# Kernel tuning notes

Measured on AMD Instinct MI355X. Metric: run time of the kernel, lower is better.

The kernel has to match this reference:

```python
import jax, jax.numpy as jnp
import numpy as np

# dims: O=1 templates/chains, L=384 residues, d_pair=d_bias=128, 4 heads x 32
O, L, DP, DB, H, DH = 1, 384, 128, 128, 4, 32
SCALING = 1.0 / np.sqrt(DH)


def _ln(x, g, b):
    # torch nn.LayerNorm over last dim, eps=1e-5, biased variance
    m = jnp.mean(x, axis=-1, keepdims=True)
    v = jnp.mean((x - m) ** 2, axis=-1, keepdims=True)
    return (x - m) * jax.lax.rsqrt(v + 1e-5) * g + b


def setup_inputs() -> dict:
    key = jax.random.key(0)
    ks = jax.random.split(key, 9)

    def w(k, shape, s=0.02):
        return (jax.random.normal(k, shape) * s).astype(jnp.float32)

    return {
        "pair": jax.random.normal(ks[0], (O, L, L, DP), dtype=jnp.float32),
        "bias": jax.random.normal(ks[1], (O, L, L, DB), dtype=jnp.float32),
        "ln_pair_g": jnp.ones((DP,), jnp.float32),
        "ln_pair_b": jnp.zeros((DP,), jnp.float32),
        "ln_bias_g": jnp.ones((DB,), jnp.float32),
        "ln_bias_b": jnp.zeros((DB,), jnp.float32),
        "Wq": w(ks[2], (H * DH, DP)),  # torch Linear weight layout (out, in)
        "Wk": w(ks[3], (H * DH, DP)),
        "Wv": w(ks[4], (H * DH, DP)),
        "Wb": w(ks[5], (H, DB)),
        "Wg": w(ks[6], (H * DH, DP)),
        "bg": jnp.ones((H * DH,), jnp.float32),
        "Wo": w(ks[7], (DP, H * DH)),
        "bo": w(ks[8], (DP,)),
    }


def reference(pair, bias, ln_pair_g, ln_pair_b, ln_bias_g, ln_bias_b,
              Wq, Wk, Wv, Wb, Wg, bg, Wo, bo):
    # is_row=True: swap the two L axes so attention runs along rows
    p = jnp.transpose(pair, (0, 2, 1, 3))   # [O, L, L, DP]
    bsrc = jnp.transpose(bias, (0, 2, 1, 3))  # [O, L, L, DB]

    p = _ln(p, ln_pair_g, ln_pair_b)
    bsrc = _ln(bsrc, ln_bias_g, ln_bias_b)

    q = (p @ Wq.T).reshape(O, L, L, H, DH) * SCALING
    k = (p @ Wk.T).reshape(O, L, L, H, DH) / L
    v = (p @ Wv.T).reshape(O, L, L, H, DH)
    b = bsrc @ Wb.T                         # [O, L, L, H] pairwise bias
    gate = jax.nn.sigmoid(p @ Wg.T + bg)    # [O, L, L, H*DH]

    # attention scores contracted over the non-attended axial dim n and head dim k
    attn = jnp.einsum('bnihk,bnjhk->bijh', q, k) + b
    attn = jax.nn.softmax(attn, axis=2)     # softmax over j (torch dim=-2)

    out = jnp.einsum('bijh,bnjhd->bnihd', attn, v).reshape(O, L, L, H * DH)
    out = (gate * out) @ Wo.T + bo          # [O, L, L, DP]
    return jnp.transpose(out, (0, 2, 1, 3))  # undo is_row permute
```

## Files before the change

kernel.cpp:

```cpp
#include <hip/hip_runtime.h>
#include <hip/hip_bf16.h>

#define L_DIM 384
#define DPC 128
#define NH 4
#define DHD 32
#define HD 128
#define NROWS (L_DIM*L_DIM)
#define NSPLIT 16

#define SB_BF16 32768
#define SB_Q 0
#define SB_K 8192
#define SB_G 16384
#define SB_V 24576

typedef __hip_bfloat16 bf16;
typedef __attribute__((ext_vector_type(8))) short bf8_t;
typedef __attribute__((ext_vector_type(4))) short bf4_t;
typedef __attribute__((ext_vector_type(4))) float f4_t;

__device__ __forceinline__ float bf2f(bf16 x){ return __bfloat162float(x); }
__device__ __forceinline__ bf16 f2bf(float x){ return __float2bfloat16(x); }

union bfu8 { bf8_t v; bf16 h[8]; };

__global__ __launch_bounds__(256) void k_prep(
    const float* __restrict__ Wq, const float* __restrict__ Wk, const float* __restrict__ Wv,
    const float* __restrict__ Wg, const float* __restrict__ Wo,
    bf16* __restrict__ Wqp, bf16* __restrict__ Wkp, bf16* __restrict__ Wvp,
    bf16* __restrict__ Wgp, bf16* __restrict__ Wop)
{
  const int o = blockIdx.x * 256 + threadIdx.x;
  const int j = o & 7, lane = (o >> 3) & 63, ks = (o >> 9) & 3, nt = o >> 11;
  const int src = (nt*16 + (lane & 15))*DPC + ks*32 + (lane >> 4)*8 + j;
  Wqp[o] = f2bf(Wq[src]);
  Wkp[o] = f2bf(Wk[src]);
  Wvp[o] = f2bf(Wv[src]);
  Wgp[o] = f2bf(Wg[src]);
  Wop[o] = f2bf(Wo[src]);
}

__global__ __launch_bounds__(256) void k_bias_proj(
    const float* __restrict__ bias, const float* __restrict__ lng, const float* __restrict__ lnb,
    const float* __restrict__ Wb, float* __restrict__ bscore)
{
  const int tid = threadIdx.x;
  const int wave = tid >> 6, lane = tid & 63;
  const int sub = lane >> 4, l16 = lane & 15, c = l16 * 8;
  const int t = blockIdx.x * 16 + wave * 4 + sub;
  const int j = t / L_DIM, i = t % L_DIM;

  const float4 ga = *(const float4*)&lng[c], gb = *(const float4*)&lng[c+4];
  const float4 ba = *(const float4*)&lnb[c], bb = *(const float4*)&lnb[c+4];
  const float4 xa = *(const float4*)&bias[(size_t)t * DPC + c];
  const float4 xb = *(const float4*)&bias[(size_t)t * DPC + c + 4];

  float s  = xa.x+xa.y+xa.z+xa.w + xb.x+xb.y+xb.z+xb.w;
  float ss = xa.x*xa.x+xa.y*xa.y+xa.z*xa.z+xa.w*xa.w
           + xb.x*xb.x+xb.y*xb.y+xb.z*xb.z+xb.w*xb.w;
  #pragma unroll
  for (int off = 8; off; off >>= 1) { s += __shfl_xor(s, off, 64); ss += __shfl_xor(ss, off, 64); }
  const float mean = s * (1.f/128.f);
  const float var  = ss * (1.f/128.f) - mean*mean;
  const float rstd = rsqrtf(var + 1e-5f);
  float y[8];
  y[0]=(xa.x-mean)*rstd*ga.x+ba.x; y[1]=(xa.y-mean)*rstd*ga.y+ba.y;
  y[2]=(xa.z-mean)*rstd*ga.z+ba.z; y[3]=(xa.w-mean)*rstd*ga.w+ba.w;
  y[4]=(xb.x-mean)*rstd*gb.x+bb.x; y[5]=(xb.y-mean)*rstd*gb.y+bb.y;
  y[6]=(xb.z-mean)*rstd*gb.z+bb.z; y[7]=(xb.w-mean)*rstd*gb.w+bb.w;

  float p[4];
  #pragma unroll
  for (int h = 0; h < 4; ++h) {
    const float4 wa = *(const float4*)&Wb[h*DPC + c];
    const float4 wb4 = *(const float4*)&Wb[h*DPC + c + 4];
    p[h] = y[0]*wa.x + y[1]*wa.y + y[2]*wa.z + y[3]*wa.w
         + y[4]*wb4.x + y[5]*wb4.y + y[6]*wb4.z + y[7]*wb4.w;
    #pragma unroll
    for (int off = 8; off; off >>= 1) p[h] += __shfl_xor(p[h], off, 64);
  }
  if (l16 == 0) {
    #pragma unroll
    for (int h = 0; h < 4; ++h)
      bscore[((size_t)h*L_DIM + i)*L_DIM + j] = p[h];
  }
}

__global__ __launch_bounds__(256, 6) void k_pair_proj(
    const float* __restrict__ pair, const float* __restrict__ lng, const float* __restrict__ lnb,
    const bf16* __restrict__ Wqp, const bf16* __restrict__ Wkp, const bf16* __restrict__ Wvp,
    const bf16* __restrict__ Wgp, const float* __restrict__ bg,
    bf16* __restrict__ fused)
{
  __shared__ __align__(16) bf16 Sh[4 * 3072];
  const int tid = threadIdx.x;
  const int wave = tid >> 6, lane = tid & 63;
  bf16* WS = Sh + wave * 3072;
  const int i6 = blockIdx.x / 384, n = blockIdx.x % 384;
  const int i0g = i6*64 + wave*16;
  const int m = lane & 15, q4 = lane >> 4;

  bf16* SB = fused + ((size_t)n*6 + i6) * SB_BF16;

  {
    const int half = lane >> 5, l32 = lane & 31, c = l32 * 4;
    const float4 g4 = *(const float4*)&lng[c];
    const float4 b4 = *(const float4*)&lnb[c];
    float4 xv[8];
    #pragma unroll
    for (int rr = 0; rr < 8; ++rr)
      xv[rr] = *(const float4*)&pair[((size_t)(i0g + rr*2 + half)*L_DIM + n)*DPC + c];
    #pragma unroll
    for (int rr = 0; rr < 8; ++rr) {
      const int r = rr*2 + half;
      float s  = xv[rr].x + xv[rr].y + xv[rr].z + xv[rr].w;
      float ss = xv[rr].x*xv[rr].x + xv[rr].y*xv[rr].y + xv[rr].z*xv[rr].z + xv[rr].w*xv[rr].w;
      #pragma unroll
      for (int off = 16; off; off >>= 1) { s += __shfl_xor(s, off, 64); ss += __shfl_xor(ss, off, 64); }
      const float mean = s * (1.f/128.f);
      const float var  = ss * (1.f/128.f) - mean*mean;
      const float rstd = rsqrtf(var + 1e-5f);
      union { bf16 h[4]; bf4_t v; } pk;
      pk.h[0] = f2bf((xv[rr].x-mean)*rstd*g4.x + b4.x);
      pk.h[1] = f2bf((xv[rr].y-mean)*rstd*g4.y + b4.y);
      pk.h[2] = f2bf((xv[rr].z-mean)*rstd*g4.z + b4.z);
      pk.h[3] = f2bf((xv[rr].w-mean)*rstd*g4.w + b4.w);
      *(bf4_t*)&WS[r*136 + c] = pk.v;
    }
  }

  bf8_t afr[4];
  #pragma unroll
  for (int ks = 0; ks < 4; ++ks)
    afr[ks] = *(const bf8_t*)&WS[m*136 + ks*32 + q4*8];

  const bf16* W3[3] = {Wqp, Wkp, Wgp};
  const int soff3[3] = {SB_Q, SB_K, SB_G};
  #pragma unroll
  for (int s3 = 0; s3 < 3; ++s3) {
    const bf16* Wp = W3[s3];
    #pragma unroll
    for (int h = 0; h < 4; ++h) {
      f4_t acc0 = {0.f,0.f,0.f,0.f}, acc1 = {0.f,0.f,0.f,0.f};
      #pragma unroll
      for (int ks = 0; ks < 4; ++ks) {
        bf8_t b0 = *(const bf8_t*)&Wp[((h*2    )*4 + ks)*512 + lane*8];
        bf8_t b1 = *(const bf8_t*)&Wp[((h*2 + 1)*4 + ks)*512 + lane*8];
        acc0 = __builtin_amdgcn_mfma_f32_16x16x32_bf16(afr[ks], b0, acc0, 0, 0, 0);
        acc1 = __builtin_amdgcn_mfma_f32_16x16x32_bf16(afr[ks], b1, acc1, 0, 0, 0);
      }
      if (s3 == 2) {
        const float bg0 = bg[h*32 + m], bg1 = bg[h*32 + 16 + m];
        #pragma unroll
        for (int reg = 0; reg < 4; ++reg) {
          acc0[reg] = 1.f / (1.f + __expf(-(acc0[reg] + bg0)));
          acc1[reg] = 1.f / (1.f + __expf(-(acc1[reg] + bg1)));
        }
      }
      #pragma unroll
      for (int reg = 0; reg < 4; ++reg) {
        WS[(q4*4 + reg)*40 + m]      = f2bf(acc0[reg]);
        WS[(q4*4 + reg)*40 + 16 + m] = f2bf(acc1[reg]);
      }
      bf8_t fv = *(const bf8_t*)&WS[m*40 + q4*8];
      *(bf8_t*)&SB[soff3[s3] + (h*4 + wave)*512 + lane*8] = fv;
    }
  }

  #pragma unroll
  for (int nt = 0; nt < 8; ++nt) {
    f4_t acc = {0.f,0.f,0.f,0.f};
    #pragma unroll
    for (int ks = 0; ks < 4; ++ks) {
      bf8_t bfr = *(const bf8_t*)&Wvp[(nt*4 + ks)*512 + lane*8];
      acc = __builtin_amdgcn_mfma_f32_16x16x32_bf16(afr[ks], bfr, acc, 0, 0, 0);
    }
    #pragma unroll
    for (int reg = 0; reg < 4; ++reg)
      WS[(nt*16 + m)*24 + q4*4 + reg] = f2bf(acc[reg]);
  }
  const int Jloc = wave >> 1;
  const int wo = (wave & 1) * 32;
  #pragma unroll
  for (int st = 0; st < 4; ++st) {
    const int fid = st*2 + (lane >> 5);
    const int h = fid >> 1, dt = fid & 1;
    const int lnl = lane & 31;
    bf8_t val = *(const bf8_t*)&WS[(h*32 + dt*16 + (lnl & 15))*24 + (lnl >> 4)*8];
    *(bf8_t*)&SB[SB_V + (((Jloc*4 + h)*2 + dt)*512) + (wo + lnl)*8] = val;
  }
}

__global__ __launch_bounds__(256) void k_qk(
    const bf16* __restrict__ fused, float* __restrict__ Spart)
{
  const int tid = threadIdx.x, wave = tid >> 6, lane = tid & 63;
  const int m = lane & 15, q4 = lane >> 4;
  const int b = blockIdx.x;
  const int ks = b / 36, rem = b % 36;
  const int h = rem / 9, t9 = rem % 9;
  const int i0 = (t9/3)*128, j0 = (t9%3)*128;
  const int wr = (wave >> 1)*64, wc = (wave & 1)*64;

  f4_t acc[4][4];
  #pragma unroll
  for (int a = 0; a < 4; ++a)
    #pragma unroll
    for (int c = 0; c < 4; ++c) acc[a][c] = (f4_t){0.f,0.f,0.f,0.f};

  const bf16* qp = fused + ((size_t)(ks*24)*6 + ((i0 + wr) >> 6))*SB_BF16
                         + SB_Q + h*2048 + (size_t)lane*8;
  const bf16* kp = fused + ((size_t)(ks*24)*6 + ((j0 + wc) >> 6))*SB_BF16
                         + SB_K + h*2048 + (size_t)lane*8;
  const size_t nstride = (size_t)6*SB_BF16;

  bf8_t af[4], bfr[4];
  #pragma unroll
  for (int x = 0; x < 4; ++x) {
    af[x]  = *(const bf8_t*)(qp + x*512);
    bfr[x] = *(const bf8_t*)(kp + x*512);
  }
  #pragma unroll 2
  for (int kt = 0; kt < 24; ++kt) {
    bf8_t afn[4], bfn[4];
    if (kt < 23) {
      const bf16* qn = qp + (size_t)(kt+1)*nstride;
      const bf16* kn = kp + (size_t)(kt+1)*nstride;
      #pragma unroll
      for (int x = 0; x < 4; ++x) {
        afn[x] = *(const bf8_t*)(qn + x*512);
        bfn[x] = *(const bf8_t*)(kn + x*512);
      }
    }
    #pragma unroll
    for (int mt = 0; mt < 4; ++mt)
      #pragma unroll
      for (int nt = 0; nt < 4; ++nt)
        acc[mt][nt] = __builtin_amdgcn_mfma_f32_16x16x32_bf16(af[mt], bfr[nt], acc[mt][nt], 0, 0, 0);
    #pragma unroll
    for (int x = 0; x < 4; ++x) { af[x] = afn[x]; bfr[x] = bfn[x]; }
  }
  float* Sp = Spart + ((size_t)(ks*NH + h)*9 + t9)*16384;
  #pragma unroll
  for (int mt = 0; mt < 4; ++mt)
    #pragma unroll
    for (int nt = 0; nt < 4; ++nt)
      #pragma unroll
      for (int reg = 0; reg < 4; ++reg) {
        int il = wr + mt*16 + q4*4 + reg;
        int jl = wc + nt*16 + m;
        Sp[il*128 + jl] = acc[mt][nt][reg];
      }
}

__global__ __launch_bounds__(192) void k_softmax(
    const float* __restrict__ Spart, const float* __restrict__ bscore, bf16* __restrict__ attnf)
{
  const int t = threadIdx.x, wave = t >> 6, lane = t & 63;
  const int h = blockIdx.x / L_DIM, i = blockIdx.x % L_DIM;
  const float sc = 0.17677669529663687f / 384.f;
  const size_t toff = ((size_t)((i >> 7)*3 + wave))*16384 + (size_t)(i & 127)*128 + (t & 63)*2;

  float ax = 0.f, ay = 0.f;
  #pragma unroll
  for (int ksp = 0; ksp < NSPLIT; ++ksp) {
    float2 p = *(const float2*)&Spart[((size_t)(ksp*NH + h)*9)*16384 + toff];
    ax += p.x; ay += p.y;
  }
  const size_t off = ((size_t)h*L_DIM + i)*L_DIM + t*2;
  const float2 bs = *(const float2*)&bscore[off];
  ax = ax*sc + bs.x;
  ay = ay*sc + bs.y;

  __shared__ float redm[3], reds[3];
  float mx = fmaxf(ax, ay);
  #pragma unroll
  for (int o = 32; o; o >>= 1) mx = fmaxf(mx, __shfl_xor(mx, o, 64));
  if (lane == 0) redm[wave] = mx;
  __syncthreads();
  mx = fmaxf(fmaxf(redm[0], redm[1]), redm[2]);
  float ex = __expf(ax - mx), ey = __expf(ay - mx);
  float sm = ex + ey;
  #pragma unroll
  for (int o = 32; o; o >>= 1) sm += __shfl_xor(sm, o, 64);
  if (lane == 0) reds[wave] = sm;
  __syncthreads();
  const float inv = 1.f / (reds[0] + reds[1] + reds[2]);

  const int j = t*2;
  const int I = i >> 4, mm = i & 15, J = j >> 5, q4 = (j >> 3) & 3, jj = j & 7;
  union { bf16 h2[2]; unsigned u; } pk;
  pk.h2[0] = f2bf(ex * inv);
  pk.h2[1] = f2bf(ey * inv);
  size_t a = ((((size_t)h*24 + I)*12 + J)*64 + q4*16 + mm)*8 + jj;
  *(unsigned*)&attnf[a] = pk.u;
}

__global__ __launch_bounds__(256) void k_pv(
    const bf16* __restrict__ attnf, const bf16* __restrict__ fused,
    bf16* __restrict__ goutf)
{
  __shared__ __align__(16) bf16 Cs2[384*40];
  const int tid = threadIdx.x, wave = tid >> 6, lane = tid & 63;
  const int m = lane & 15, q4 = lane >> 4;
  const int n = blockIdx.x >> 2, h = blockIdx.x & 3;

  bf8_t ugp[6];
  #pragma unroll
  for (int it = 0; it < 6; ++it) {
    int u = tid + it*256;
    int I = u >> 6, ln = u & 63;
    ugp[it] = *(const bf8_t*)&fused[((size_t)n*6 + (I>>2))*SB_BF16 + SB_G
                                    + (h*4 + (I&3))*512 + ln*8];
  }

  f4_t acc[6][2];
  #pragma unroll
  for (int a = 0; a < 6; ++a) { acc[a][0] = (f4_t){0,0,0,0}; acc[a][1] = (f4_t){0,0,0,0}; }

  for (int J = 0; J < 12; ++J) {
    const bf16* vb = fused + ((size_t)n*6 + (J>>1))*SB_BF16 + SB_V
                           + (((J&1)*4 + h)*2)*512;
    bf8_t b0 = *(const bf8_t*)&vb[lane*8];
    bf8_t b1 = *(const bf8_t*)&vb[512 + lane*8];
    #pragma unroll
    for (int mt = 0; mt < 6; ++mt) {
      const int I = wave*6 + mt;
      bf8_t af = *(const bf8_t*)&attnf[(((size_t)h*24 + I)*12 + J)*512 + (size_t)lane*8];
      acc[mt][0] = __builtin_amdgcn_mfma_f32_16x16x32_bf16(af, b0, acc[mt][0], 0, 0, 0);
      acc[mt][1] = __builtin_amdgcn_mfma_f32_16x16x32_bf16(af, b1, acc[mt][1], 0, 0, 0);
    }
  }
  #pragma unroll
  for (int mt = 0; mt < 6; ++mt)
    #pragma unroll
    for (int dt = 0; dt < 2; ++dt)
      #pragma unroll
      for (int reg = 0; reg < 4; ++reg) {
        int i_loc = 16*(wave*6 + mt) + q4*4 + reg;
        Cs2[i_loc*40 + dt*16 + m] = f2bf(acc[mt][dt][reg]);
      }
  __syncthreads();
  #pragma unroll
  for (int it = 0; it < 6; ++it) {
    int u = tid + it*256;
    int I = u >> 6, ln = u & 63;
    bfu8 uc, ug, uo;
    uc.v = *(const bf8_t*)&Cs2[(I*16 + (ln&15))*40 + (ln>>4)*8];
    ug.v = ugp[it];
    #pragma unroll
    for (int e = 0; e < 8; ++e) uo.h[e] = f2bf(bf2f(uc.h[e]) * bf2f(ug.h[e]));
    size_t gidx = ((((size_t)n*24 + I)*NH + h)*64 + ln)*8;
    *(bf8_t*)&goutf[gidx] = uo.v;
  }
}

__global__ __launch_bounds__(256) void k_out(
    const bf16* __restrict__ goutf, const bf16* __restrict__ Wop, const float* __restrict__ bo,
    float* __restrict__ outp)
{
  __shared__ __align__(16) float Cs[64][132];
  const int tid = threadIdx.x, wave = tid >> 6, lane = tid & 63;
  const int m = lane & 15, q4 = lane >> 4;
  const int i0 = (blockIdx.x / 384) * 64, n = blockIdx.x % 384;

  bf8_t afr[4];
  #pragma unroll
  for (int ks = 0; ks < 4; ++ks)
    afr[ks] = *(const bf8_t*)&goutf[((((size_t)n*24 + (i0>>4) + wave)*NH + ks)*64 + lane)*8];

  #pragma unroll
  for (int nt = 0; nt < 8; ++nt) {
    f4_t acc = {0.f, 0.f, 0.f, 0.f};
    #pragma unroll
    for (int ks = 0; ks < 4; ++ks) {
      bf8_t bfr = *(const bf8_t*)&Wop[(nt*4 + ks)*512 + lane*8];
      acc = __builtin_amdgcn_mfma_f32_16x16x32_bf16(afr[ks], bfr, acc, 0, 0, 0);
    }
    const int col = nt*16 + m;
    const float bov = bo[col];
    #pragma unroll
    for (int reg = 0; reg < 4; ++reg)
      Cs[wave*16 + q4*4 + reg][col] = acc[reg] + bov;
  }
  __syncthreads();
  for (int u = tid; u < 2048; u += 256) {
    int r = u >> 5, c4 = (u & 31) * 4;
    size_t off = ((size_t)(i0 + r)*L_DIM + n)*DPC + c4;
    *(float4*)&outp[off] = *(const float4*)&Cs[r][c4];
  }
}

extern "C" void kernel_launch(void* const* d_in, const int* in_sizes, int n_in,
                              void* d_out, int out_size, void* d_ws, size_t ws_size,
                              hipStream_t stream)
{
  (void)in_sizes; (void)n_in; (void)out_size; (void)ws_size;
  const float* pair = (const float*)d_in[0];
  const float* bias = (const float*)d_in[1];
  const float* lnpg = (const float*)d_in[2];
  const float* lnpb = (const float*)d_in[3];
  const float* lnbg = (const float*)d_in[4];
  const float* lnbb = (const float*)d_in[5];
  const float* Wq   = (const float*)d_in[6];
  const float* Wk   = (const float*)d_in[7];
  const float* Wv   = (const float*)d_in[8];
  const float* Wb   = (const float*)d_in[9];
  const float* Wg   = (const float*)d_in[10];
  const float* bg   = (const float*)d_in[11];
  const float* Wo   = (const float*)d_in[12];
  const float* bo   = (const float*)d_in[13];
  float* outp = (float*)d_out;

  char* ws = (char*)d_ws;
  const size_t FUSED_SZ = (size_t)2304 * SB_BF16 * 2;
  bf16* fusedb  = (bf16*)(ws);
  float* bscore = (float*)(ws + FUSED_SZ);
  float* Spart  = (float*)(ws + FUSED_SZ + (size_t)NH*L_DIM*L_DIM*4);
  bf16*  attnf  = (bf16*)(ws + FUSED_SZ + (size_t)NH*L_DIM*L_DIM*4
                             + (size_t)NSPLIT*NH*L_DIM*L_DIM*4);
  char*  wb     = ws + FUSED_SZ + (size_t)NH*L_DIM*L_DIM*4
                     + (size_t)NSPLIT*NH*L_DIM*L_DIM*4 + (size_t)NH*L_DIM*L_DIM*2;
  bf16* Wqp = (bf16*)(wb);
  bf16* Wkp = (bf16*)(wb + 32768);
  bf16* Wvp = (bf16*)(wb + 65536);
  bf16* Wgp = (bf16*)(wb + 98304);
  bf16* Wop = (bf16*)(wb + 131072);
  bf16* goutf = (bf16*)Spart;

  hipLaunchKernelGGL(k_prep, dim3(64), dim3(256), 0, stream, Wq, Wk, Wv, Wg, Wo,
                     Wqp, Wkp, Wvp, Wgp, Wop);
  hipLaunchKernelGGL(k_bias_proj, dim3(NROWS/16), dim3(256), 0, stream, bias, lnbg, lnbb, Wb, bscore);
  hipLaunchKernelGGL(k_pair_proj, dim3(NROWS/64), dim3(256), 0, stream, pair, lnpg, lnpb,
                     Wqp, Wkp, Wvp, Wgp, bg, fusedb);
  hipLaunchKernelGGL(k_qk, dim3(NSPLIT*36), dim3(256), 0, stream, fusedb, Spart);
  hipLaunchKernelGGL(k_softmax, dim3(NH*L_DIM), dim3(192), 0, stream, Spart, bscore, attnf);
  hipLaunchKernelGGL(k_pv, dim3(L_DIM*NH), dim3(256), 0, stream, attnf, fusedb, goutf);
  hipLaunchKernelGGL(k_out, dim3(NROWS/64), dim3(256), 0, stream, goutf, Wop, bo, outp);
}
```

Measured before the change: 397.3 us.

## Make pair projection persistent with per-wave register-resident weights

```diff
diff --git a/kernel.cpp b/kernel.cpp
--- a/kernel.cpp
+++ b/kernel.cpp
@@ -87,108 +87,124 @@
   }
 }
 
-__global__ __launch_bounds__(256, 6) void k_pair_proj(
+__global__ __launch_bounds__(256, 2) void k_pair_proj(
     const float* __restrict__ pair, const float* __restrict__ lng, const float* __restrict__ lnb,
     const bf16* __restrict__ Wqp, const bf16* __restrict__ Wkp, const bf16* __restrict__ Wvp,
     const bf16* __restrict__ Wgp, const float* __restrict__ bg,
     bf16* __restrict__ fused)
 {
-  __shared__ __align__(16) bf16 Sh[4 * 3072];
+  __shared__ __align__(16) bf16 As[64*136];
+  __shared__ __align__(16) bf16 Chunk[3*640];
+  __shared__ __align__(16) bf16 CT[128*72];
   const int tid = threadIdx.x;
   const int wave = tid >> 6, lane = tid & 63;
-  bf16* WS = Sh + wave * 3072;
-  const int i6 = blockIdx.x / 384, n = blockIdx.x % 384;
-  const int i0g = i6*64 + wave*16;
   const int m = lane & 15, q4 = lane >> 4;
 
-  bf16* SB = fused + ((size_t)n*6 + i6) * SB_BF16;
-
-  {
-    const int half = lane >> 5, l32 = lane & 31, c = l32 * 4;
-    const float4 g4 = *(const float4*)&lng[c];
-    const float4 b4 = *(const float4*)&lnb[c];
-    float4 xv[8];
-    #pragma unroll
-    for (int rr = 0; rr < 8; ++rr)
-      xv[rr] = *(const float4*)&pair[((size_t)(i0g + rr*2 + half)*L_DIM + n)*DPC + c];
-    #pragma unroll
-    for (int rr = 0; rr < 8; ++rr) {
-      const int r = rr*2 + half;
-      float s  = xv[rr].x + xv[rr].y + xv[rr].z + xv[rr].w;
-      float ss = xv[rr].x*xv[rr].x + xv[rr].y*xv[rr].y + xv[rr].z*xv[rr].z + xv[rr].w*xv[rr].w;
-      #pragma unroll
-      for (int off = 16; off; off >>= 1) { s += __shfl_xor(s, off, 64); ss += __shfl_xor(ss, off, 64); }
-      const float mean = s * (1.f/128.f);
-      const float var  = ss * (1.f/128.f) - mean*mean;
-      const float rstd = rsqrtf(var + 1e-5f);
-      union { bf16 h[4]; bf4_t v; } pk;
-      pk.h[0] = f2bf((xv[rr].x-mean)*rstd*g4.x + b4.x);
-      pk.h[1] = f2bf((xv[rr].y-mean)*rstd*g4.y + b4.y);
-      pk.h[2] = f2bf((xv[rr].z-mean)*rstd*g4.z + b4.z);
-      pk.h[3] = f2bf((xv[rr].w-mean)*rstd*g4.w + b4.w);
-      *(bf4_t*)&WS[r*136 + c] = pk.v;
+  const bf16* Wp = (wave == 0) ? Wqp : (wave == 1) ? Wkp : (wave == 2) ? Wgp : Wvp;
+  bf8_t wfr[32];
+  #pragma unroll
+  for (int f = 0; f < 32; ++f)
+    wfr[f] = *(const bf8_t*)&Wp[f*512 + lane*8];
+
+  const float bg0 = bg[((wave == 2) ? 0 : 0)];
+  (void)bg0;
+
+  for (int t = blockIdx.x; t < 2304; t += 576) {
+    const int i6 = t / 384, n = t % 384;
+    const int i0g = i6*64 + wave*16;
+    bf16* SB = fused + ((size_t)n*6 + i6) * SB_BF16;
+
+    {
+      const int half = lane >> 5, l32 = lane & 31, c = l32 * 4;
+      const float4 g4 = *(const float4*)&lng[c];
+      const float4 b4 = *(const float4*)&lnb[c];
+      float4 xv[8];
+      #pragma unroll
+      for (int rr = 0; rr < 8; ++rr)
+        xv[rr] = *(const float4*)&pair[((size_t)(i0g + rr*2 + half)*L_DIM + n)*DPC + c];
+      #pragma unroll
+      for (int rr = 0; rr < 8; ++rr) {
+        const int r = rr*2 + half;
+        float s  = xv[rr].x + xv[rr].y + xv[rr].z + xv[rr].w;
+        float ss = xv[rr].x*xv[rr].x + xv[rr].y*xv[rr].y + xv[rr].z*xv[rr].z + xv[rr].w*xv[rr].w;
+        #pragma unroll
+        for (int off = 16; off; off >>= 1) { s += __shfl_xor(s, off, 64); ss += __shfl_xor(ss, off, 64); }
+        const float mean = s * (1.f/128.f);
+        const float var  = ss * (1.f/128.f) - mean*mean;
+        const float rstd = rsqrtf(var + 1e-5f);
+        union { bf16 h[4]; bf4_t v; } pk;
+        pk.h[0] = f2bf((xv[rr].x-mean)*rstd*g4.x + b4.x);
+        pk.h[1] = f2bf((xv[rr].y-mean)*rstd*g4.y + b4.y);
+        pk.h[2] = f2bf((xv[rr].z-mean)*rstd*g4.z + b4.z);
+        pk.h[3] = f2bf((xv[rr].w-mean)*rstd*g4.w + b4.w);
+        *(bf4_t*)&As[(wave*16 + r)*136 + c] = pk.v;
+      }
     }
-  }
-
-  bf8_t afr[4];
-  #pragma unroll
-  for (int ks = 0; ks < 4; ++ks)
-    afr[ks] = *(const bf8_t*)&WS[m*136 + ks*32 + q4*8];
-
-  const bf16* W3[3] = {Wqp, Wkp, Wgp};
-  const int soff3[3] = {SB_Q, SB_K, SB_G};
-  #pragma unroll
-  for (int s3 = 0; s3 < 3; ++s3) {
-    const bf16* Wp = W3[s3];
-    #pragma unroll
-    for (int h = 0; h < 4; ++h) {
-      f4_t acc0 = {0.f,0.f,0.f,0.f}, acc1 = {0.f,0.f,0.f,0.f};
-      #pragma unroll
-      for (int ks = 0; ks < 4; ++ks) {
-        bf8_t b0 = *(const bf8_t*)&Wp[((h*2    )*4 + ks)*512 + lane*8];
-        bf8_t b1 = *(const bf8_t*)&Wp[((h*2 + 1)*4 + ks)*512 + lane*8];
-        acc0 = __builtin_amdgcn_mfma_f32_16x16x32_bf16(afr[ks], b0, acc0, 0, 0, 0);
-        acc1 = __builtin_amdgcn_mfma_f32_16x16x32_bf16(afr[ks], b1, acc1, 0, 0, 0);
-      }
-      if (s3 == 2) {
-        const float bg0 = bg[h*32 + m], bg1 = bg[h*32 + 16 + m];
-        #pragma unroll
-        for (int reg = 0; reg < 4; ++reg) {
-          acc0[reg] = 1.f / (1.f + __expf(-(acc0[reg] + bg0)));
-          acc1[reg] = 1.f / (1.f + __expf(-(acc1[reg] + bg1)));
+    __syncthreads();
+
+    if (wave < 3) {
+      const int soff = (wave == 0) ? SB_Q : (wave == 1) ? SB_K : SB_G;
+      bf16* CH = Chunk + wave*640;
+      #pragma unroll
+      for (int I = 0; I < 4; ++I) {
+        bf8_t afr[4];
+        #pragma unroll
+        for (int ks = 0; ks < 4; ++ks)
+          afr[ks] = *(const bf8_t*)&As[(I*16 + m)*136 + ks*32 + q4*8];
+        #pragma unroll
+        for (int h = 0; h < 4; ++h) {
+          f4_t acc0 = {0.f,0.f,0.f,0.f}, acc1 = {0.f,0.f,0.f,0.f};
+          #pragma unroll
+          for (int ks = 0; ks < 4; ++ks) {
+            acc0 = __builtin_amdgcn_mfma_f32_16x16x32_bf16(afr[ks], wfr[(h*2    )*4 + ks], acc0, 0, 0, 0);
+            acc1 = __builtin_amdgcn_mfma_f32_16x16x32_bf16(afr[ks], wfr[(h*2 + 1)*4 + ks], acc1, 0, 0, 0);
+          }
+          if (wave == 2) {
+            const float b0v = bg[h*32 + m], b1v = bg[h*32 + 16 + m];
+            #pragma unroll
+            for (int reg = 0; reg < 4; ++reg) {
+              acc0[reg] = 1.f / (1.f + __expf(-(acc0[reg] + b0v)));
+              acc1[reg] = 1.f / (1.f + __expf(-(acc1[reg] + b1v)));
+            }
+          }
+          #pragma unroll
+          for (int reg = 0; reg < 4; ++reg) {
+            CH[(q4*4 + reg)*40 + m]      = f2bf(acc0[reg]);
+            CH[(q4*4 + reg)*40 + 16 + m] = f2bf(acc1[reg]);
+          }
+          bf8_t fv = *(const bf8_t*)&CH[m*40 + q4*8];
+          *(bf8_t*)&SB[soff + (h*4 + I)*512 + lane*8] = fv;
         }
       }
-      #pragma unroll
-      for (int reg = 0; reg < 4; ++reg) {
-        WS[(q4*4 + reg)*40 + m]      = f2bf(acc0[reg]);
-        WS[(q4*4 + reg)*40 + 16 + m] = f2bf(acc1[reg]);
-      }
-      bf8_t fv = *(const bf8_t*)&WS[m*40 + q4*8];
-      *(bf8_t*)&SB[soff3[s3] + (h*4 + wave)*512 + lane*8] = fv;
+    } else {
+      #pragma unroll
+      for (int I = 0; I < 4; ++I) {
+        bf8_t afr[4];
+        #pragma unroll
+        for (int ks = 0; ks < 4; ++ks)
+          afr[ks] = *(const bf8_t*)&As[(I*16 + m)*136 + ks*32 + q4*8];
+        #pragma unroll
+        for (int nt = 0; nt < 8; ++nt) {
+          f4_t acc = {0.f,0.f,0.f,0.f};
+          #pragma unroll
+          for (int ks = 0; ks < 4; ++ks)
+            acc = __builtin_amdgcn_mfma_f32_16x16x32_bf16(afr[ks], wfr[nt*4 + ks], acc, 0, 0, 0);
+          #pragma unroll
+          for (int reg = 0; reg < 4; ++reg)
+            CT[(nt*16 + m)*72 + I*16 + q4*4 + reg] = f2bf(acc[reg]);
+        }
+      }
+      #pragma unroll
+      for (int J = 0; J < 2; ++J)
+        #pragma unroll
+        for (int h = 0; h < 4; ++h)
+          #pragma unroll
+          for (int dt = 0; dt < 2; ++dt) {
+            bf8_t val = *(const bf8_t*)&CT[(h*32 + dt*16 + (lane & 15))*72 + J*32 + (lane >> 4)*8];
+            *(bf8_t*)&SB[SB_V + ((J*4 + h)*2 + dt)*512 + lane*8] = val;
+          }
     }
-  }
-
-  #pragma unroll
-  for (int nt = 0; nt < 8; ++nt) {
-    f4_t acc = {0.f,0.f,0.f,0.f};
-    #pragma unroll
-    for (int ks = 0; ks < 4; ++ks) {
-      bf8_t bfr = *(const bf8_t*)&Wvp[(nt*4 + ks)*512 + lane*8];
-      acc = __builtin_amdgcn_mfma_f32_16x16x32_bf16(afr[ks], bfr, acc, 0, 0, 0);
-    }
-    #pragma unroll
-    for (int reg = 0; reg < 4; ++reg)
-      WS[(nt*16 + m)*24 + q4*4 + reg] = f2bf(acc[reg]);
-  }
-  const int Jloc = wave >> 1;
-  const int wo = (wave & 1) * 32;
-  #pragma unroll
-  for (int st = 0; st < 4; ++st) {
-    const int fid = st*2 + (lane >> 5);
-    const int h = fid >> 1, dt = fid & 1;
-    const int lnl = lane & 31;
-    bf8_t val = *(const bf8_t*)&WS[(h*32 + dt*16 + (lnl & 15))*24 + (lnl >> 4)*8];
-    *(bf8_t*)&SB[SB_V + (((Jloc*4 + h)*2 + dt)*512) + (wo + lnl)*8] = val;
+    __syncthreads();
   }
 }
 
@@ -432,7 +448,7 @@
   hipLaunchKernelGGL(k_prep, dim3(64), dim3(256), 0, stream, Wq, Wk, Wv, Wg, Wo,
                      Wqp, Wkp, Wvp, Wgp, Wop);
   hipLaunchKernelGGL(k_bias_proj, dim3(NROWS/16), dim3(256), 0, stream, bias, lnbg, lnbb, Wb, bscore);
-  hipLaunchKernelGGL(k_pair_proj, dim3(NROWS/64), dim3(256), 0, stream, pair, lnpg, lnpb,
+  hipLaunchKernelGGL(k_pair_proj, dim3(576), dim3(256), 0, stream, pair, lnpg, lnpb,
                      Wqp, Wkp, Wvp, Wgp, bg, fusedb);
   hipLaunchKernelGGL(k_qk, dim3(NSPLIT*36), dim3(256), 0, stream, fusedb, Spart);
   hipLaunchKernelGGL(k_softmax, dim3(NH*L_DIM), dim3(192), 0, stream, Spart, bscore, attnf);
```

Result: slower. 430.7 us (+8.4%).
